# Kernel optimization log

Measured on AMD Instinct MI355X. Metric: run time of the kernel, lower is better.

The kernel has to match this reference:

```python
import jax, jax.numpy as jnp
import numpy as np

B, L, D, H = 2, 2048, 1024, 16
DPH = D // H  # 64
EPS = 1e-5


def setup_inputs() -> dict:
    rng = jax.random.key(0)
    ks = jax.random.split(rng, 16)
    init = lambda k, shape: (jax.random.normal(k, shape, dtype=jnp.float32) * 0.02)
    return {
        "key": jax.random.normal(ks[0], (B, L, D), dtype=jnp.float32),
        "value": jax.random.normal(ks[1], (B, L, D), dtype=jnp.float32),
        "query": jax.random.normal(ks[2], (B, L, D), dtype=jnp.float32),
        "Wq": init(ks[3], (D, D)), "bq": jnp.zeros((D,), jnp.float32),
        "Wk": init(ks[4], (D, D)), "bk": jnp.zeros((D,), jnp.float32),
        "Wv": init(ks[5], (D, D)), "bv": jnp.zeros((D,), jnp.float32),
        "Wo": init(ks[6], (D, D)), "bo": jnp.zeros((D,), jnp.float32),
        "gamma": jnp.ones((D,), jnp.float32),
        "beta": jnp.zeros((D,), jnp.float32),
    }


def reference(key, value, query, Wq, bq, Wk, bk, Wv, bv, Wo, bo, gamma, beta):
    residual_in = query
    # torch Linear: x @ W.T + b
    k = key @ Wk.T + bk
    v = value @ Wv.T + bv
    q = query @ Wq.T + bq
    # faithful to source: flat view into (B*H, L, DPH) WITHOUT head transpose
    k = k.reshape(B * H, L, DPH)
    v = v.reshape(B * H, L, DPH)
    q = q.reshape(B * H, L, DPH)
    # faithful quirky scale: (dim_per_head // num_heads) ** -0.5
    scale = (DPH // H) ** (-0.5)
    scores = jnp.einsum("bqd,bkd->bqk", q, k) * scale  # [B*H, L, L]
    attention = jax.nn.softmax(scores, axis=2)
    context = jnp.einsum("bqk,bkd->bqd", attention, v)  # [B*H, L, DPH]
    context = context.reshape(B, L, D)
    output = context @ Wo.T + bo
    x = residual_in + output
    mean = jnp.mean(x, axis=-1, keepdims=True)
    var = jnp.var(x, axis=-1, keepdims=True)
    output = (x - mean) * jax.lax.rsqrt(var + EPS) * gamma + beta
    return (output, attention)
```

## Files before the change

kernel.cpp:

```cpp
#include <hip/hip_runtime.h>
#include <cstddef>
#include <cstdint>

#define Lseq   2048
#define Dmodel 1024
#define NGRP   32
#define MROWS  4096
#define EPS_LN 1e-5f

typedef short  s16x8 __attribute__((ext_vector_type(8)));
typedef float  f32x4 __attribute__((ext_vector_type(4)));
typedef unsigned short ushort_t;

__device__ __forceinline__ ushort_t f2bf(float f) {
    union { float f; unsigned u; } v; v.f = f;
    unsigned r = v.u + 0x7FFFu + ((v.u >> 16) & 1u);
    return (ushort_t)(r >> 16);
}

__device__ __forceinline__ void gld16(const ushort_t* g, ushort_t* lds) {
    __builtin_amdgcn_global_load_lds(
        (const __attribute__((address_space(1))) unsigned int*)(uintptr_t)g,
        (__attribute__((address_space(3))) unsigned int*)(uintptr_t)lds,
        16, 0, 0);
}

struct CvtArgs {
    const float* src[7];
    ushort_t*    dst[7];
    int          n8[7];
};

__global__ __launch_bounds__(256) void cvt_bf16(CvtArgs a)
{
    const int ti = blockIdx.y;
    const float* __restrict__ s = a.src[ti];
    ushort_t* __restrict__    d = a.dst[ti];
    const int n8 = a.n8[ti];
    for (int i = blockIdx.x * 256 + threadIdx.x; i < n8; i += gridDim.x * 256) {
        float4 x0 = reinterpret_cast<const float4*>(s)[i * 2];
        float4 x1 = reinterpret_cast<const float4*>(s)[i * 2 + 1];
        s16x8 o;
        o[0]=f2bf(x0.x); o[1]=f2bf(x0.y); o[2]=f2bf(x0.z); o[3]=f2bf(x0.w);
        o[4]=f2bf(x1.x); o[5]=f2bf(x1.y); o[6]=f2bf(x1.z); o[7]=f2bf(x1.w);
        reinterpret_cast<s16x8*>(d)[i] = o;
    }
}

template<bool OUT_BF16>
__device__ __forceinline__ void gemm_body(
    const ushort_t* __restrict__ A, const ushort_t* __restrict__ W,
    const float* __restrict__ bias, const float* __restrict__ resid,
    void* __restrict__ outv, ushort_t* As, ushort_t* Bs)
{
    const int t  = threadIdx.x;
    const int m0 = blockIdx.y * 128;
    const int n0 = blockIdx.x * 64;
    const int w  = t >> 6;
    const int l  = t & 63;
    const int lr = l & 15;
    const int lg = l >> 4;
    const int wm = w >> 1, wn = w & 1;

    const ushort_t* ga0 = A + (size_t)(m0 + w * 32 + (l >> 2)) * 1024 + (l & 3) * 8;
    const ushort_t* ga1 = ga0 + (size_t)16 * 1024;
    const ushort_t* gb0 = W + (size_t)(n0 + w * 16 + (l >> 2)) * 1024 + (l & 3) * 8;
    ushort_t* la0 = &As[(w * 32) * 32];
    ushort_t* la1 = &As[(w * 32 + 16) * 32];
    ushort_t* lb0 = &Bs[(w * 16) * 32];

    f32x4 acc[4][2] = {};

    for (int k0 = 0; k0 < 1024; k0 += 32) {
        gld16(ga0 + k0, la0);
        gld16(ga1 + k0, la1);
        gld16(gb0 + k0, lb0);
        __syncthreads();

        s16x8 af[4], bf[2];
#pragma unroll
        for (int mi = 0; mi < 4; ++mi)
            af[mi] = *reinterpret_cast<const s16x8*>(&As[(wm * 64 + mi * 16 + lr) * 32 + lg * 8]);
#pragma unroll
        for (int ni = 0; ni < 2; ++ni)
            bf[ni] = *reinterpret_cast<const s16x8*>(&Bs[(wn * 32 + ni * 16 + lr) * 32 + lg * 8]);
#pragma unroll
        for (int mi = 0; mi < 4; ++mi)
#pragma unroll
            for (int ni = 0; ni < 2; ++ni)
                acc[mi][ni] = __builtin_amdgcn_mfma_f32_16x16x32_bf16(af[mi], bf[ni], acc[mi][ni], 0, 0, 0);
        __syncthreads();
    }

#pragma unroll
    for (int mi = 0; mi < 4; ++mi)
#pragma unroll
        for (int ni = 0; ni < 2; ++ni)
#pragma unroll
            for (int r = 0; r < 4; ++r) {
                int row = m0 + wm * 64 + mi * 16 + lg * 4 + r;
                int col = n0 + wn * 32 + ni * 16 + lr;
                float v = acc[mi][ni][r] + bias[col];
                if (OUT_BF16) {
                    ((ushort_t*)outv)[(size_t)row * 1024 + col] = f2bf(v);
                } else {
                    v += resid[(size_t)row * 1024 + col];
                    ((float*)outv)[(size_t)row * 1024 + col] = v;
                }
            }
}

struct QkvArgs {
    const ushort_t* A[3];
    const ushort_t* W[3];
    const float*    bias[3];
    ushort_t*       out[3];
};

__global__ __launch_bounds__(256) void gemm_qkv(QkvArgs a)
{
    __shared__ ushort_t As[128 * 32];
    __shared__ ushort_t Bs[64 * 32];
    const int z = blockIdx.z;
    gemm_body<true>(a.A[z], a.W[z], a.bias[z], nullptr, a.out[z], As, Bs);
}

__global__ __launch_bounds__(256) void gemm_o(
    const ushort_t* __restrict__ A, const ushort_t* __restrict__ W,
    const float* __restrict__ bias, const float* __restrict__ resid,
    float* __restrict__ out)
{
    __shared__ ushort_t As[128 * 32];
    __shared__ ushort_t Bs[64 * 32];
    gemm_body<false>(A, W, bias, resid, out, As, Bs);
}

__global__ __launch_bounds__(256) void transpose_v(
    const ushort_t* __restrict__ vb, ushort_t* __restrict__ vt)
{
    __shared__ ushort_t tile[64][72];
    const int g  = blockIdx.x;
    const int lt = blockIdx.y;
    const int t  = threadIdx.x;
#pragma unroll
    for (int it = 0; it < 2; ++it) {
        int s = t * 2 + it, row = s >> 3, sub = (s & 7) * 8;
        *reinterpret_cast<s16x8*>(&tile[row][sub]) =
            *reinterpret_cast<const s16x8*>(vb + ((size_t)(g*2048 + lt*64 + row))*64 + sub);
    }
    __syncthreads();
#pragma unroll
    for (int it = 0; it < 2; ++it) {
        int s = t * 2 + it, drow = s >> 3, sub = (s & 7) * 8;
        s16x8 o;
#pragma unroll
        for (int j = 0; j < 8; ++j) o[j] = (short)tile[sub + j][drow];
        *reinterpret_cast<s16x8*>(vt + ((size_t)(g*64 + drow))*2048 + lt*64 + sub) = o;
    }
}

__global__ __launch_bounds__(256) void attn_stats(
    const ushort_t* __restrict__ qb, const ushort_t* __restrict__ kb,
    float* __restrict__ invb)
{
    __shared__ ushort_t Ks[2][64][72];

    const int g  = blockIdx.x;
    const int r0 = blockIdx.y * 128;
    const int t  = threadIdx.x;
    const int w  = t >> 6;
    const int l  = t & 63;
    const int lr = l & 15;
    const int lg = l >> 4;
    const int srow0 = (t*2)   >> 3, ssub0 = ((t*2)   & 7) * 8;
    const int srow1 = (t*2+1) >> 3, ssub1 = ((t*2+1) & 7) * 8;

    s16x8 qf[2][2];
#pragma unroll
    for (int rf = 0; rf < 2; ++rf) {
        const ushort_t* qrow = qb + ((size_t)(g*2048 + r0 + w*32 + rf*16 + lr)) * 64;
        qf[rf][0] = *reinterpret_cast<const s16x8*>(qrow + lg*8);
        qf[rf][1] = *reinterpret_cast<const s16x8*>(qrow + 32 + lg*8);
    }

    *reinterpret_cast<s16x8*>(&Ks[0][srow0][ssub0]) =
        *reinterpret_cast<const s16x8*>(kb + ((size_t)(g*2048 + srow0))*64 + ssub0);
    *reinterpret_cast<s16x8*>(&Ks[0][srow1][ssub1]) =
        *reinterpret_cast<const s16x8*>(kb + ((size_t)(g*2048 + srow1))*64 + ssub1);
    __syncthreads();

    float lsum[2][4] = {};
    int cur = 0;

    for (int jc = 0; jc < 32; ++jc) {
        s16x8 nk0, nk1;
        if (jc < 31) {
            nk0 = *reinterpret_cast<const s16x8*>(kb + ((size_t)(g*2048 + (jc+1)*64 + srow0))*64 + ssub0);
            nk1 = *reinterpret_cast<const s16x8*>(kb + ((size_t)(g*2048 + (jc+1)*64 + srow1))*64 + ssub1);
        }
#pragma unroll
        for (int jf = 0; jf < 4; ++jf) {
            s16x8 b0 = *reinterpret_cast<const s16x8*>(&Ks[cur][jf*16 + lr][lg*8]);
            s16x8 b1 = *reinterpret_cast<const s16x8*>(&Ks[cur][jf*16 + lr][32 + lg*8]);
#pragma unroll
            for (int rf = 0; rf < 2; ++rf) {
                f32x4 sv = {};
                sv = __builtin_amdgcn_mfma_f32_16x16x32_bf16(qf[rf][0], b0, sv, 0, 0, 0);
                sv = __builtin_amdgcn_mfma_f32_16x16x32_bf16(qf[rf][1], b1, sv, 0, 0, 0);
#pragma unroll
                for (int r = 0; r < 4; ++r)
                    lsum[rf][r] += __expf(sv[r] * 0.5f);
            }
        }
        if (jc < 31) {
            *reinterpret_cast<s16x8*>(&Ks[cur^1][srow0][ssub0]) = nk0;
            *reinterpret_cast<s16x8*>(&Ks[cur^1][srow1][ssub1]) = nk1;
        }
        __syncthreads();
        cur ^= 1;
    }

#pragma unroll
    for (int rf = 0; rf < 2; ++rf)
#pragma unroll
        for (int r = 0; r < 4; ++r) {
            float v = lsum[rf][r];
            v += __shfl_xor(v, 1); v += __shfl_xor(v, 2);
            v += __shfl_xor(v, 4); v += __shfl_xor(v, 8);
            if (lr == 0)
                invb[(size_t)g*2048 + r0 + w*32 + rf*16 + lg*4 + r] = 1.f / v;
        }
}

__global__ __launch_bounds__(256) void attn_main(
    const ushort_t* __restrict__ qb, const ushort_t* __restrict__ kb,
    const ushort_t* __restrict__ vt, const float* __restrict__ invb,
    float* __restrict__ attn, ushort_t* __restrict__ ctxb)
{
    __shared__ ushort_t Ks[2][64][72];
    __shared__ ushort_t Vs[2][64][72];
    __shared__ ushort_t Ps[64][72];

    const int g  = blockIdx.x;
    const int r0 = blockIdx.y * 64;
    const int t  = threadIdx.x;
    const int w  = t >> 6;
    const int l  = t & 63;
    const int lr = l & 15;
    const int lg = l >> 4;
    const int srow0 = (t*2)   >> 3, ssub0 = ((t*2)   & 7) * 8;
    const int srow1 = (t*2+1) >> 3, ssub1 = ((t*2+1) & 7) * 8;

    s16x8 qf0, qf1;
    {
        const ushort_t* qrow = qb + ((size_t)(g*2048 + r0 + w*16 + lr)) * 64;
        qf0 = *reinterpret_cast<const s16x8*>(qrow + lg*8);
        qf1 = *reinterpret_cast<const s16x8*>(qrow + 32 + lg*8);
    }

    float inv[4];
#pragma unroll
    for (int r = 0; r < 4; ++r)
        inv[r] = invb[(size_t)g*2048 + r0 + w*16 + lg*4 + r];

    *reinterpret_cast<s16x8*>(&Ks[0][srow0][ssub0]) =
        *reinterpret_cast<const s16x8*>(kb + ((size_t)(g*2048 + srow0))*64 + ssub0);
    *reinterpret_cast<s16x8*>(&Ks[0][srow1][ssub1]) =
        *reinterpret_cast<const s16x8*>(kb + ((size_t)(g*2048 + srow1))*64 + ssub1);
    *reinterpret_cast<s16x8*>(&Vs[0][srow0][ssub0]) =
        *reinterpret_cast<const s16x8*>(vt + ((size_t)(g*64 + srow0))*2048 + ssub0);
    *reinterpret_cast<s16x8*>(&Vs[0][srow1][ssub1]) =
        *reinterpret_cast<const s16x8*>(vt + ((size_t)(g*64 + srow1))*2048 + ssub1);
    __syncthreads();

    f32x4 ctx[4] = {};
    int cur = 0;

    for (int jc = 0; jc < 32; ++jc) {
        s16x8 nk0, nk1, nv0, nv1;
        if (jc < 31) {
            nk0 = *reinterpret_cast<const s16x8*>(kb + ((size_t)(g*2048 + (jc+1)*64 + srow0))*64 + ssub0);
            nk1 = *reinterpret_cast<const s16x8*>(kb + ((size_t)(g*2048 + (jc+1)*64 + srow1))*64 + ssub1);
            nv0 = *reinterpret_cast<const s16x8*>(vt + ((size_t)(g*64 + srow0))*2048 + (jc+1)*64 + ssub0);
            nv1 = *reinterpret_cast<const s16x8*>(vt + ((size_t)(g*64 + srow1))*2048 + (jc+1)*64 + ssub1);
        }

#pragma unroll
        for (int jf = 0; jf < 4; ++jf) {
            s16x8 b0 = *reinterpret_cast<const s16x8*>(&Ks[cur][jf*16 + lr][lg*8]);
            s16x8 b1 = *reinterpret_cast<const s16x8*>(&Ks[cur][jf*16 + lr][32 + lg*8]);
            f32x4 s = {};
            s = __builtin_amdgcn_mfma_f32_16x16x32_bf16(qf0, b0, s, 0, 0, 0);
            s = __builtin_amdgcn_mfma_f32_16x16x32_bf16(qf1, b1, s, 0, 0, 0);
#pragma unroll
            for (int r = 0; r < 4; ++r) {
                float e = __expf(s[r] * 0.5f);
                attn[(size_t)g*Lseq*Lseq + (size_t)(r0 + w*16 + lg*4 + r)*Lseq
                     + jc*64 + jf*16 + lr] = e * inv[r];
                Ps[w*16 + lg*4 + r][jf*16 + lr] = f2bf(e);
            }
        }

#pragma unroll
        for (int kk = 0; kk < 2; ++kk) {
            s16x8 pa = *reinterpret_cast<const s16x8*>(&Ps[w*16 + lr][kk*32 + lg*8]);
#pragma unroll
            for (int ni = 0; ni < 4; ++ni) {
                s16x8 bv = *reinterpret_cast<const s16x8*>(&Vs[cur][ni*16 + lr][kk*32 + lg*8]);
                ctx[ni] = __builtin_amdgcn_mfma_f32_16x16x32_bf16(pa, bv, ctx[ni], 0, 0, 0);
            }
        }

        if (jc < 31) {
            *reinterpret_cast<s16x8*>(&Ks[cur^1][srow0][ssub0]) = nk0;
            *reinterpret_cast<s16x8*>(&Ks[cur^1][srow1][ssub1]) = nk1;
            *reinterpret_cast<s16x8*>(&Vs[cur^1][srow0][ssub0]) = nv0;
            *reinterpret_cast<s16x8*>(&Vs[cur^1][srow1][ssub1]) = nv1;
        }
        __syncthreads();
        cur ^= 1;
    }

#pragma unroll
    for (int ni = 0; ni < 4; ++ni)
#pragma unroll
        for (int r = 0; r < 4; ++r) {
            int l2 = r0 + w*16 + lg*4 + r;
            int d2 = ni*16 + lr;
            ctxb[(size_t)g*Lseq*64 + (size_t)l2*64 + d2] = f2bf(ctx[ni][r] * inv[r]);
        }
}

__global__ __launch_bounds__(256) void ln_kernel(
    float* __restrict__ x, const float* __restrict__ gamma,
    const float* __restrict__ beta, float* __restrict__ out)
{
    const int row = blockIdx.x;
    const int t   = threadIdx.x;
    const int c   = t * 4;

    float4 v = *reinterpret_cast<const float4*>(x + (size_t)row * Dmodel + c);
    float s  = v.x + v.y + v.z + v.w;
    float s2 = v.x*v.x + v.y*v.y + v.z*v.z + v.w*v.w;
    for (int off = 1; off < 64; off <<= 1) {
        s  += __shfl_xor(s, off);
        s2 += __shfl_xor(s2, off);
    }
    __shared__ float ssum[4], ssum2[4];
    int wid = t >> 6;
    if ((t & 63) == 0) { ssum[wid] = s; ssum2[wid] = s2; }
    __syncthreads();
    s  = ssum[0] + ssum[1] + ssum[2] + ssum[3];
    s2 = ssum2[0] + ssum2[1] + ssum2[2] + ssum2[3];

    float mean = s * (1.f / Dmodel);
    float var  = s2 * (1.f / Dmodel) - mean * mean;
    float rstd = rsqrtf(var + EPS_LN);

    float4 gv = *reinterpret_cast<const float4*>(gamma + c);
    float4 bv = *reinterpret_cast<const float4*>(beta + c);
    float4 o;
    o.x = (v.x - mean) * rstd * gv.x + bv.x;
    o.y = (v.y - mean) * rstd * gv.y + bv.y;
    o.z = (v.z - mean) * rstd * gv.z + bv.z;
    o.w = (v.w - mean) * rstd * gv.w + bv.w;
    *reinterpret_cast<float4*>(out + (size_t)row * Dmodel + c) = o;
}

extern "C" void kernel_launch(void* const* d_in, const int* in_sizes, int n_in,
                              void* d_out, int out_size, void* d_ws, size_t ws_size,
                              hipStream_t stream)
{
    const float* key   = (const float*)d_in[0];
    const float* value = (const float*)d_in[1];
    const float* query = (const float*)d_in[2];
    const float* Wq    = (const float*)d_in[3];
    const float* bq    = (const float*)d_in[4];
    const float* Wk    = (const float*)d_in[5];
    const float* bk    = (const float*)d_in[6];
    const float* Wv    = (const float*)d_in[7];
    const float* bv    = (const float*)d_in[8];
    const float* Wo    = (const float*)d_in[9];
    const float* bo    = (const float*)d_in[10];
    const float* gamma = (const float*)d_in[11];
    const float* beta  = (const float*)d_in[12];

    float* out  = (float*)d_out;
    float* attn = out + (size_t)MROWS * Dmodel;

    const size_t M1 = 1024 * 1024;
    ushort_t* ws   = (ushort_t*)d_ws;
    ushort_t* qb   = ws;
    ushort_t* kb   = ws + 4  * M1;
    ushort_t* vb   = ws + 8  * M1;
    ushort_t* vt   = ws + 12 * M1;
    ushort_t* qx   = ws + 16 * M1;
    ushort_t* kx   = ws + 20 * M1;
    ushort_t* vx   = ws + 24 * M1;
    ushort_t* wqx  = ws + 28 * M1;
    ushort_t* wkx  = ws + 29 * M1;
    ushort_t* wvx  = ws + 30 * M1;
    ushort_t* wox  = ws + 31 * M1;
    ushort_t* ctxb = qx;
    float*    invb = (float*)kx;

    CvtArgs ca;
    ca.src[0]=query; ca.dst[0]=qx;  ca.n8[0]=(int)(4*M1/8);
    ca.src[1]=key;   ca.dst[1]=kx;  ca.n8[1]=(int)(4*M1/8);
    ca.src[2]=value; ca.dst[2]=vx;  ca.n8[2]=(int)(4*M1/8);
    ca.src[3]=Wq;    ca.dst[3]=wqx; ca.n8[3]=(int)(M1/8);
    ca.src[4]=Wk;    ca.dst[4]=wkx; ca.n8[4]=(int)(M1/8);
    ca.src[5]=Wv;    ca.dst[5]=wvx; ca.n8[5]=(int)(M1/8);
    ca.src[6]=Wo;    ca.dst[6]=wox; ca.n8[6]=(int)(M1/8);
    cvt_bf16<<<dim3(512, 7), 256, 0, stream>>>(ca);

    QkvArgs qa;
    qa.A[0]=qx; qa.W[0]=wqx; qa.bias[0]=bq; qa.out[0]=qb;
    qa.A[1]=kx; qa.W[1]=wkx; qa.bias[1]=bk; qa.out[1]=kb;
    qa.A[2]=vx; qa.W[2]=wvx; qa.bias[2]=bv; qa.out[2]=vb;
    gemm_qkv<<<dim3(Dmodel/64, MROWS/128, 3), 256, 0, stream>>>(qa);

    transpose_v<<<dim3(NGRP, Lseq/64), 256, 0, stream>>>(vb, vt);

    attn_stats<<<dim3(NGRP, Lseq/128), 256, 0, stream>>>(qb, kb, invb);

    attn_main<<<dim3(NGRP, Lseq/64), 256, 0, stream>>>(qb, kb, vt, invb, attn, ctxb);

    gemm_o<<<dim3(Dmodel/64, MROWS/128), 256, 0, stream>>>(ctxb, wox, bo, query, out);

    ln_kernel<<<dim3(MROWS), 256, 0, stream>>>(out, gamma, beta, out);
}
```

Baseline: 335.2 us.

## Transpose score MFMA for vectorized attention stores and widen GEMM tiles to 128x128

In the attention kernel the score MFMA operands are swapped so each lane holds four consecutive key columns of one query row. This turns the scalar attention-probability writes into 16-byte vector stores and the P tile writes into packed bf16 stores via v_cvt_pk_bf16_f32. The projection GEMMs move from 128x64 to 128x128 block tiles with a 4x4 MFMA accumulator per wave, improving operand reuse but halving grid size and raising register and LDS use. The context normalization now reloads per-row inverse sums from global memory at the epilogue.

```diff
diff --git a/kernel.cpp b/kernel.cpp
--- a/kernel.cpp
+++ b/kernel.cpp
@@ -16,6 +16,12 @@
     union { float f; unsigned u; } v; v.f = f;
     unsigned r = v.u + 0x7FFFu + ((v.u >> 16) & 1u);
     return (ushort_t)(r >> 16);
+}
+
+__device__ __forceinline__ unsigned cvt_pk_bf16(float lo, float hi) {
+    unsigned r;
+    asm("v_cvt_pk_bf16_f32 %0, %1, %2" : "=v"(r) : "v"(lo), "v"(hi));
+    return r;
 }
 
 __device__ __forceinline__ void gld16(const ushort_t* g, ushort_t* lds) {
@@ -55,39 +61,42 @@
 {
     const int t  = threadIdx.x;
     const int m0 = blockIdx.y * 128;
-    const int n0 = blockIdx.x * 64;
+    const int n0 = blockIdx.x * 128;
     const int w  = t >> 6;
     const int l  = t & 63;
     const int lr = l & 15;
     const int lg = l >> 4;
     const int wm = w >> 1, wn = w & 1;
 
-    const ushort_t* ga0 = A + (size_t)(m0 + w * 32 + (l >> 2)) * 1024 + (l & 3) * 8;
-    const ushort_t* ga1 = ga0 + (size_t)16 * 1024;
-    const ushort_t* gb0 = W + (size_t)(n0 + w * 16 + (l >> 2)) * 1024 + (l & 3) * 8;
-    ushort_t* la0 = &As[(w * 32) * 32];
-    ushort_t* la1 = &As[(w * 32 + 16) * 32];
-    ushort_t* lb0 = &Bs[(w * 16) * 32];
-
-    f32x4 acc[4][2] = {};
+    const ushort_t* gA  = A + (size_t)(m0 + w * 32 + (l >> 2)) * 1024 + (l & 3) * 8;
+    const ushort_t* gA2 = gA + (size_t)16 * 1024;
+    const ushort_t* gB  = W + (size_t)(n0 + w * 32 + (l >> 2)) * 1024 + (l & 3) * 8;
+    const ushort_t* gB2 = gB + (size_t)16 * 1024;
+    ushort_t* lA  = &As[(w * 32) * 32];
+    ushort_t* lA2 = &As[(w * 32 + 16) * 32];
+    ushort_t* lB  = &Bs[(w * 32) * 32];
+    ushort_t* lB2 = &Bs[(w * 32 + 16) * 32];
+
+    f32x4 acc[4][4] = {};
 
     for (int k0 = 0; k0 < 1024; k0 += 32) {
-        gld16(ga0 + k0, la0);
-        gld16(ga1 + k0, la1);
-        gld16(gb0 + k0, lb0);
+        gld16(gA  + k0, lA);
+        gld16(gA2 + k0, lA2);
+        gld16(gB  + k0, lB);
+        gld16(gB2 + k0, lB2);
         __syncthreads();
 
-        s16x8 af[4], bf[2];
+        s16x8 af[4], bf[4];
 #pragma unroll
         for (int mi = 0; mi < 4; ++mi)
             af[mi] = *reinterpret_cast<const s16x8*>(&As[(wm * 64 + mi * 16 + lr) * 32 + lg * 8]);
 #pragma unroll
-        for (int ni = 0; ni < 2; ++ni)
-            bf[ni] = *reinterpret_cast<const s16x8*>(&Bs[(wn * 32 + ni * 16 + lr) * 32 + lg * 8]);
+        for (int ni = 0; ni < 4; ++ni)
+            bf[ni] = *reinterpret_cast<const s16x8*>(&Bs[(wn * 64 + ni * 16 + lr) * 32 + lg * 8]);
 #pragma unroll
         for (int mi = 0; mi < 4; ++mi)
 #pragma unroll
-            for (int ni = 0; ni < 2; ++ni)
+            for (int ni = 0; ni < 4; ++ni)
                 acc[mi][ni] = __builtin_amdgcn_mfma_f32_16x16x32_bf16(af[mi], bf[ni], acc[mi][ni], 0, 0, 0);
         __syncthreads();
     }
@@ -95,11 +104,11 @@
 #pragma unroll
     for (int mi = 0; mi < 4; ++mi)
 #pragma unroll
-        for (int ni = 0; ni < 2; ++ni)
+        for (int ni = 0; ni < 4; ++ni)
 #pragma unroll
             for (int r = 0; r < 4; ++r) {
                 int row = m0 + wm * 64 + mi * 16 + lg * 4 + r;
-                int col = n0 + wn * 32 + ni * 16 + lr;
+                int col = n0 + wn * 64 + ni * 16 + lr;
                 float v = acc[mi][ni][r] + bias[col];
                 if (OUT_BF16) {
                     ((ushort_t*)outv)[(size_t)row * 1024 + col] = f2bf(v);
@@ -120,7 +129,7 @@
 __global__ __launch_bounds__(256) void gemm_qkv(QkvArgs a)
 {
     __shared__ ushort_t As[128 * 32];
-    __shared__ ushort_t Bs[64 * 32];
+    __shared__ ushort_t Bs[128 * 32];
     const int z = blockIdx.z;
     gemm_body<true>(a.A[z], a.W[z], a.bias[z], nullptr, a.out[z], As, Bs);
 }
@@ -131,7 +140,7 @@
     float* __restrict__ out)
 {
     __shared__ ushort_t As[128 * 32];
-    __shared__ ushort_t Bs[64 * 32];
+    __shared__ ushort_t Bs[128 * 32];
     gemm_body<false>(A, W, bias, resid, out, As, Bs);
 }
 
@@ -258,10 +267,8 @@
         qf1 = *reinterpret_cast<const s16x8*>(qrow + 32 + lg*8);
     }
 
-    float inv[4];
-#pragma unroll
-    for (int r = 0; r < 4; ++r)
-        inv[r] = invb[(size_t)g*2048 + r0 + w*16 + lg*4 + r];
+    const float inv_s = invb[(size_t)g*2048 + r0 + w*16 + lr];
+    float* arow = attn + (size_t)g*Lseq*Lseq + (size_t)(r0 + w*16 + lr)*Lseq + lg*4;
 
     *reinterpret_cast<s16x8*>(&Ks[0][srow0][ssub0]) =
         *reinterpret_cast<const s16x8*>(kb + ((size_t)(g*2048 + srow0))*64 + ssub0);
@@ -287,18 +294,25 @@
 
 #pragma unroll
         for (int jf = 0; jf < 4; ++jf) {
-            s16x8 b0 = *reinterpret_cast<const s16x8*>(&Ks[cur][jf*16 + lr][lg*8]);
-            s16x8 b1 = *reinterpret_cast<const s16x8*>(&Ks[cur][jf*16 + lr][32 + lg*8]);
+            s16x8 a0 = *reinterpret_cast<const s16x8*>(&Ks[cur][jf*16 + lr][lg*8]);
+            s16x8 a1 = *reinterpret_cast<const s16x8*>(&Ks[cur][jf*16 + lr][32 + lg*8]);
             f32x4 s = {};
-            s = __builtin_amdgcn_mfma_f32_16x16x32_bf16(qf0, b0, s, 0, 0, 0);
-            s = __builtin_amdgcn_mfma_f32_16x16x32_bf16(qf1, b1, s, 0, 0, 0);
-#pragma unroll
-            for (int r = 0; r < 4; ++r) {
-                float e = __expf(s[r] * 0.5f);
-                attn[(size_t)g*Lseq*Lseq + (size_t)(r0 + w*16 + lg*4 + r)*Lseq
-                     + jc*64 + jf*16 + lr] = e * inv[r];
-                Ps[w*16 + lg*4 + r][jf*16 + lr] = f2bf(e);
-            }
+            s = __builtin_amdgcn_mfma_f32_16x16x32_bf16(a0, qf0, s, 0, 0, 0);
+            s = __builtin_amdgcn_mfma_f32_16x16x32_bf16(a1, qf1, s, 0, 0, 0);
+
+            float e0 = __expf(s[0] * 0.5f);
+            float e1 = __expf(s[1] * 0.5f);
+            float e2 = __expf(s[2] * 0.5f);
+            float e3 = __expf(s[3] * 0.5f);
+
+            f32x4 o;
+            o[0] = e0 * inv_s; o[1] = e1 * inv_s; o[2] = e2 * inv_s; o[3] = e3 * inv_s;
+            *reinterpret_cast<f32x4*>(arow + jc*64 + jf*16) = o;
+
+            unsigned p01 = cvt_pk_bf16(e0, e1);
+            unsigned p23 = cvt_pk_bf16(e2, e3);
+            uint2 pk; pk.x = p01; pk.y = p23;
+            *reinterpret_cast<uint2*>(&Ps[w*16 + lr][jf*16 + lg*4]) = pk;
         }
 
 #pragma unroll
@@ -321,14 +335,17 @@
         cur ^= 1;
     }
 
-#pragma unroll
-    for (int ni = 0; ni < 4; ++ni)
-#pragma unroll
-        for (int r = 0; r < 4; ++r) {
-            int l2 = r0 + w*16 + lg*4 + r;
-            int d2 = ni*16 + lr;
-            ctxb[(size_t)g*Lseq*64 + (size_t)l2*64 + d2] = f2bf(ctx[ni][r] * inv[r]);
-        }
+    {
+#pragma unroll
+        for (int ni = 0; ni < 4; ++ni)
+#pragma unroll
+            for (int r = 0; r < 4; ++r) {
+                int l2 = r0 + w*16 + lg*4 + r;
+                int d2 = ni*16 + lr;
+                float iv = invb[(size_t)g*2048 + l2];
+                ctxb[(size_t)g*Lseq*64 + (size_t)l2*64 + d2] = f2bf(ctx[ni][r] * iv);
+            }
+    }
 }
 
 __global__ __launch_bounds__(256) void ln_kernel(
@@ -418,7 +435,7 @@
     qa.A[0]=qx; qa.W[0]=wqx; qa.bias[0]=bq; qa.out[0]=qb;
     qa.A[1]=kx; qa.W[1]=wkx; qa.bias[1]=bk; qa.out[1]=kb;
     qa.A[2]=vx; qa.W[2]=wvx; qa.bias[2]=bv; qa.out[2]=vb;
-    gemm_qkv<<<dim3(Dmodel/64, MROWS/128, 3), 256, 0, stream>>>(qa);
+    gemm_qkv<<<dim3(Dmodel/128, MROWS/128, 3), 256, 0, stream>>>(qa);
 
     transpose_v<<<dim3(NGRP, Lseq/64), 256, 0, stream>>>(vb, vt);
 
@@ -426,7 +443,7 @@
 
     attn_main<<<dim3(NGRP, Lseq/64), 256, 0, stream>>>(qb, kb, vt, invb, attn, ctxb);
 
-    gemm_o<<<dim3(Dmodel/64, MROWS/128), 256, 0, stream>>>(ctxb, wox, bo, query, out);
+    gemm_o<<<dim3(Dmodel/128, MROWS/128), 256, 0, stream>>>(ctxb, wox, bo, query, out);
 
     ln_kernel<<<dim3(MROWS), 256, 0, stream>>>(out, gamma, beta, out);
 }
```

After: 306.7 us. 1.09x faster.
